# Performance work log

Measured on AMD Instinct MI355X. Metric: run time of the kernel, lower is better.

## Reference

```python
import jax, jax.numpy as jnp
import numpy as np

B, T, C = 4, 2048, 1024
H, D = 16, 64  # n_head, head_dim; H*D == C
EPS = 1e-12


def _l2norm(x):
    # matches torch F.normalize(dim=-1): x / max(||x||_2, eps)
    n = jnp.sqrt(jnp.sum(x * x, axis=-1, keepdims=True))
    return x / jnp.maximum(n, EPS)


def setup_inputs() -> dict:
    key = jax.random.key(0)
    ks = jax.random.split(key, 8)
    s = 0.02
    return {
        "x": jax.random.normal(ks[0], (B, T, C), dtype=jnp.float32),
        "Wq": jax.random.normal(ks[1], (C, C), dtype=jnp.float32) * s,
        "Wk": jax.random.normal(ks[2], (C, C), dtype=jnp.float32) * s,
        "Wv": jax.random.normal(ks[3], (C, C), dtype=jnp.float32) * s,
        "Wbeta": jax.random.normal(ks[4], (H, C), dtype=jnp.float32) * s,
        "bbeta": jnp.zeros((H,), dtype=jnp.float32),
        "Wgate": jax.random.normal(ks[5], (C, C), dtype=jnp.float32) * s,
        "Wo": jax.random.normal(ks[6], (C, C), dtype=jnp.float32) * s,
    }


def _forward(x, Wq, Wk, Wv, Wbeta, bbeta, Wgate, Wo):
    q = (x @ Wq.T).reshape(B, T, H, D)
    k = (x @ Wk.T).reshape(B, T, H, D)
    v = (x @ Wv.T).reshape(B, T, H, D)
    beta = jax.nn.sigmoid(x @ Wbeta.T + bbeta)  # (B,T,H)
    gate = jax.nn.sigmoid(x @ Wgate.T)          # (B,T,C)

    q = _l2norm(q)
    k = _l2norm(k)

    # time-major for scan: (T,B,H,D) / (T,B,H)
    qT = jnp.transpose(q, (1, 0, 2, 3))
    kT = jnp.transpose(k, (1, 0, 2, 3))
    vT = jnp.transpose(v, (1, 0, 2, 3))
    bT = jnp.transpose(beta, (1, 0, 2))

    M0 = jnp.zeros((B, H, D, D), dtype=x.dtype)

    def step(M, inp):
        q_t, k_t, v_t, b_t = inp
        o_t = jnp.einsum('bhdc,bhc->bhd', M, q_t)       # read state with q (pre-update)
        Mk = jnp.einsum('bhdc,bhc->bhd', M, k_t)
        dv = v_t - Mk                                    # delta-rule error
        M = M + b_t[..., None, None] * jnp.einsum('bhd,bhc->bhdc', dv, k_t)
        return M, o_t

    _, oT = jax.lax.scan(step, M0, (qT, kT, vT, bT))     # oT: (T,B,H,D)
    o = jnp.transpose(oT, (1, 0, 2, 3)).reshape(B, T, C)
    return (gate * o) @ Wo.T


def reference(x, Wq, Wk, Wv, Wbeta, bbeta, Wgate, Wo):
    return _forward(x, Wq, Wk, Wv, Wbeta, bbeta, Wgate, Wo)
```

## Files before the change

kernel.cpp:

```cpp
#include <hip/hip_runtime.h>
#include <cstdint>
#include <cstddef>

#define Bz 4
#define Tz 2048
#define Cz 1024
#define Hz 16
#define Dz 64
#define NTOK (Bz*Tz)
#define CHL 32
#define NCH (Tz/CHL)

typedef __attribute__((ext_vector_type(8))) short  short8;
typedef __attribute__((ext_vector_type(4))) float  floatx4;

__device__ __forceinline__ unsigned short f2bf(float x) {
  union { float f; uint32_t u; } a; a.f = x;
  uint32_t r = a.u + 0x7fffu + ((a.u >> 16) & 1u);
  return (unsigned short)(r >> 16);
}
__device__ __forceinline__ float bf2f(unsigned short u) {
  union { uint32_t i; float f; } a; a.i = ((uint32_t)u) << 16; return a.f;
}
__device__ __forceinline__ float sigmoidf_(float z) {
  return 1.0f / (1.0f + __expf(-z));
}

__device__ __forceinline__ void gload_lds16(const void* gptr, void* lptr) {
  __builtin_amdgcn_global_load_lds(
      (const __attribute__((address_space(1))) void*)(uintptr_t)gptr,
      (__attribute__((address_space(3))) void*)(uint32_t)(uintptr_t)lptr,
      16, 0, 0);
}

template<int CTRL>
__device__ __forceinline__ float dpp_addf(float x) {
  int y = __builtin_amdgcn_update_dpp(0, __float_as_int(x), CTRL, 0xF, 0xF, true);
  return x + __int_as_float(y);
}
__device__ __forceinline__ float rowsum16(float x) {
  x = dpp_addf<0xB1>(x);
  x = dpp_addf<0x4E>(x);
  x = dpp_addf<0x124>(x);
  x = dpp_addf<0x128>(x);
  return x;
}

union FragU { uint32_t u[4]; short8 s; };

__global__ __launch_bounds__(256) void cvt_bf16_kernel(const float* __restrict__ in,
                                                       unsigned short* __restrict__ out,
                                                       int n4) {
  int i = blockIdx.x * blockDim.x + threadIdx.x;
  int stride = gridDim.x * blockDim.x;
  const float4* in4 = (const float4*)in;
  ushort4* out4 = (ushort4*)out;
  for (; i < n4; i += stride) {
    float4 f = in4[i];
    ushort4 u;
    u.x = f2bf(f.x); u.y = f2bf(f.y); u.z = f2bf(f.z); u.w = f2bf(f.w);
    out4[i] = u;
  }
}

__global__ __launch_bounds__(256) void cvt_w5_kernel(
    const float* __restrict__ s0, const float* __restrict__ s1,
    const float* __restrict__ s2, const float* __restrict__ s3,
    const float* __restrict__ s4,
    unsigned short* __restrict__ d0, unsigned short* __restrict__ d1,
    unsigned short* __restrict__ d2, unsigned short* __restrict__ d3,
    unsigned short* __restrict__ d4, int n4)
{
  const int w = blockIdx.y;
  const float* s = (w == 0) ? s0 : (w == 1) ? s1 : (w == 2) ? s2 : (w == 3) ? s3 : s4;
  unsigned short* d = (w == 0) ? d0 : (w == 1) ? d1 : (w == 2) ? d2 : (w == 3) ? d3 : d4;
  int i = blockIdx.x * blockDim.x + threadIdx.x;
  if (i < n4) {
    float4 f = ((const float4*)s)[i];
    ushort4 u;
    u.x = f2bf(f.x); u.y = f2bf(f.y); u.z = f2bf(f.z); u.w = f2bf(f.w);
    ((ushort4*)d)[i] = u;
  }
}

__global__ __launch_bounds__(256) void gemm_bt_kernel(
    const unsigned short* __restrict__ A,
    const unsigned short* __restrict__ W0, const unsigned short* __restrict__ W1,
    const unsigned short* __restrict__ W2, const unsigned short* __restrict__ W3,
    void* __restrict__ O0, void* __restrict__ O1,
    void* __restrict__ O2, void* __restrict__ O3,
    int M, int N, int K, int nz_sigmoid, int norm_mask, int out_bf16)
{
  const int z = blockIdx.z;
  const unsigned short* Bw = (z == 0) ? W0 : (z == 1) ? W1 : (z == 2) ? W2 : W3;
  void* Cw = (z == 0) ? O0 : (z == 1) ? O1 : (z == 2) ? O2 : O3;
  const bool act = (z == nz_sigmoid);
  const bool donorm = (norm_mask >> z) & 1;

  __shared__ unsigned short As[128 * 32];
  __shared__ unsigned short Bs[128 * 32];

  const int tid  = threadIdx.x;
  const int wid  = tid >> 6;
  const int lane = tid & 63;
  const int wm = wid & 1, wn = wid >> 1;
  const int m0 = blockIdx.y * 128;
  const int n0 = blockIdx.x * 128;

  const int srow = tid >> 2;
  const int scol = (tid & 3) * 8;

  floatx4 acc[4][4];
#pragma unroll
  for (int i = 0; i < 4; ++i)
#pragma unroll
    for (int j = 0; j < 4; ++j)
      acc[i][j] = floatx4{0.f, 0.f, 0.f, 0.f};

  const int ml = lane & 15;
  const int kq = lane >> 4;

  const unsigned short* Arow0 = A  + (size_t)(m0 + srow) * K + scol;
  const unsigned short* Arow1 = A  + (size_t)(m0 + 64 + srow) * K + scol;
  const unsigned short* Brow0 = Bw + (size_t)(n0 + srow) * K + scol;
  const unsigned short* Brow1 = Bw + (size_t)(n0 + 64 + srow) * K + scol;

  for (int kt = 0; kt < K; kt += 32) {
    gload_lds16(Arow0 + kt, &As[wid * 512]);
    gload_lds16(Arow1 + kt, &As[2048 + wid * 512]);
    gload_lds16(Brow0 + kt, &Bs[wid * 512]);
    gload_lds16(Brow1 + kt, &Bs[2048 + wid * 512]);
    __syncthreads();

    short8 af[4], bfv[4];
#pragma unroll
    for (int i = 0; i < 4; ++i) {
      af[i]  = *(const short8*)&As[(wm * 64 + i * 16 + ml) * 32 + kq * 8];
      bfv[i] = *(const short8*)&Bs[(wn * 64 + i * 16 + ml) * 32 + kq * 8];
    }
#pragma unroll
    for (int i = 0; i < 4; ++i)
#pragma unroll
      for (int j = 0; j < 4; ++j)
        acc[i][j] = __builtin_amdgcn_mfma_f32_16x16x32_bf16(af[i], bfv[j], acc[i][j], 0, 0, 0);
    __syncthreads();
  }

  float scale[4][4];
  if (donorm) {
#pragma unroll
    for (int i = 0; i < 4; ++i) {
#pragma unroll
      for (int r = 0; r < 4; ++r) {
        float ss = 0.f;
#pragma unroll
        for (int j = 0; j < 4; ++j) ss = fmaf(acc[i][j][r], acc[i][j][r], ss);
        ss = rowsum16(ss);
        scale[i][r] = 1.0f / fmaxf(sqrtf(ss), 1e-12f);
      }
    }
  }

  const int row_base = m0 + wm * 64;
  const int col_base = n0 + wn * 64;
#pragma unroll
  for (int i = 0; i < 4; ++i) {
#pragma unroll
    for (int j = 0; j < 4; ++j) {
      int col = col_base + j * 16 + ml;
#pragma unroll
      for (int r = 0; r < 4; ++r) {
        int row = row_base + i * 16 + kq * 4 + r;
        float val = acc[i][j][r];
        if (donorm) val *= scale[i][r];
        if (act) val = sigmoidf_(val);
        if (out_bf16) ((unsigned short*)Cw)[(size_t)row * N + col] = f2bf(val);
        else          ((float*)Cw)[(size_t)row * N + col] = val;
      }
    }
  }
}

__global__ __launch_bounds__(256) void beta_kernel(
    const float* __restrict__ x, const float* __restrict__ Wb,
    const float* __restrict__ bb, float* __restrict__ beta_out)
{
  const int n = blockIdx.x;
  const int wid = threadIdx.x >> 6;
  const int lane = threadIdx.x & 63;
  const float* xr = x + (size_t)n * Cz;
  for (int h = wid; h < Hz; h += 4) {
    const float* wr = Wb + (size_t)h * Cz;
    float s = 0.f;
#pragma unroll 4
    for (int i = lane; i < Cz; i += 64) s = fmaf(xr[i], wr[i], s);
#pragma unroll
    for (int ofs = 32; ofs >= 1; ofs >>= 1) s += __shfl_xor(s, ofs);
    if (lane == 0) beta_out[(size_t)n * Hz + h] = sigmoidf_(s + bb[h]);
  }
}


__global__ __launch_bounds__(256) void deltachunk_phase1(
    const unsigned short* __restrict__ qb, const unsigned short* __restrict__ kb,
    const unsigned short* __restrict__ vb, const float* __restrict__ betaf,
    float* __restrict__ of,
    unsigned short* __restrict__ qtb, unsigned short* __restrict__ wbuf,
    unsigned short* __restrict__ ubuf, unsigned short* __restrict__ ktb)
{
  __shared__ unsigned short Kb[32][72], Qb[32][72], Vb[32][72];
  __shared__ float As[32][33];
  __shared__ unsigned short Sb[32][40];
  __shared__ unsigned short Us[32][72], Ws[32][72], Qts[32][72];
  __shared__ float bsh[32];

  const int bid = blockIdx.x;
  const int chain = bid & 63;
  const int chunk = bid >> 6;
  const int b = chain >> 4, h = chain & 15;
  const int tid = threadIdx.x;
  const int wid = tid >> 6, lane = tid & 63;
  const int ml = lane & 15, kq = lane >> 4;

  const size_t tok0 = (size_t)b * Tz + (size_t)chunk * CHL;
  const size_t cb = ((size_t)chain * NCH + chunk) * 2048;

  {
    const int row = tid >> 3, c8 = (tid & 7) * 8;
    const size_t ga = (tok0 + row) * Cz + h * Dz + c8;
    *(uint4*)&Qb[row][c8] = *(const uint4*)&qb[ga];
    *(uint4*)&Kb[row][c8] = *(const uint4*)&kb[ga];
    *(uint4*)&Vb[row][c8] = *(const uint4*)&vb[ga];
  }
  if (tid < 32) bsh[tid] = betaf[(tok0 + tid) * Hz + h];
  __syncthreads();

  {
    const int tr = wid & 1, tc = wid >> 1;
    floatx4 accA = {0.f,0.f,0.f,0.f}, accS = {0.f,0.f,0.f,0.f};
#pragma unroll
    for (int eh = 0; eh < 2; ++eh) {
      short8 ka = *(const short8*)&Kb[tr * 16 + ml][eh * 32 + kq * 8];
      short8 kbf = *(const short8*)&Kb[tc * 16 + ml][eh * 32 + kq * 8];
      short8 qa = *(const short8*)&Qb[tr * 16 + ml][eh * 32 + kq * 8];
      accA = __builtin_amdgcn_mfma_f32_16x16x32_bf16(ka, kbf, accA, 0, 0, 0);
      accS = __builtin_amdgcn_mfma_f32_16x16x32_bf16(qa, kbf, accS, 0, 0, 0);
    }
#pragma unroll
    for (int r = 0; r < 4; ++r) {
      int t = tr * 16 + kq * 4 + r;
      int s = tc * 16 + ml;
      As[t][s] = bsh[t] * accA[r];
      Sb[t][s] = (t > s) ? f2bf(accS[r]) : (unsigned short)0;
    }
  }
  __syncthreads();

  if (tid < 128) {
    const int j = tid;
    float x[32];
    if (j < 64) {
#pragma unroll
      for (int t = 0; t < 32; ++t) x[t] = bsh[t] * bf2f(Vb[t][j]);
    } else {
#pragma unroll
      for (int t = 0; t < 32; ++t) x[t] = bsh[t] * bf2f(Kb[t][j - 64]);
    }
#pragma unroll
    for (int t = 0; t < 31; ++t) {
      float xt = x[t];
#pragma unroll
      for (int s = t + 1; s < 32; ++s) x[s] = fmaf(-As[s][t], xt, x[s]);
    }
    if (j < 64) {
#pragma unroll
      for (int t = 0; t < 32; ++t) Us[t][j] = f2bf(x[t]);
    } else {
#pragma unroll
      for (int t = 0; t < 32; ++t) Ws[t][j - 64] = f2bf(x[t]);
    }
  }
  __syncthreads();

  {
    const int dw = wid * 16 + ml;
    FragU bu, bw;
#pragma unroll
    for (int r = 0; r < 4; ++r) {
      bu.u[r] = (uint32_t)Us[kq * 8 + 2 * r][dw] | ((uint32_t)Us[kq * 8 + 2 * r + 1][dw] << 16);
      bw.u[r] = (uint32_t)Ws[kq * 8 + 2 * r][dw] | ((uint32_t)Ws[kq * 8 + 2 * r + 1][dw] << 16);
    }
    floatx4 accO[2], accQ[2];
#pragma unroll
    for (int tt = 0; tt < 2; ++tt) { accO[tt] = floatx4{0.f,0.f,0.f,0.f}; accQ[tt] = floatx4{0.f,0.f,0.f,0.f}; }
#pragma unroll
    for (int tt = 0; tt < 2; ++tt) {
      short8 sa = *(const short8*)&Sb[tt * 16 + ml][kq * 8];
      accO[tt] = __builtin_amdgcn_mfma_f32_16x16x32_bf16(sa, bu.s, accO[tt], 0, 0, 0);
      accQ[tt] = __builtin_amdgcn_mfma_f32_16x16x32_bf16(sa, bw.s, accQ[tt], 0, 0, 0);
    }
#pragma unroll
    for (int tt = 0; tt < 2; ++tt) {
#pragma unroll
      for (int r = 0; r < 4; ++r) {
        int t = tt * 16 + kq * 4 + r;
        of[(tok0 + t) * Cz + h * Dz + dw] = accO[tt][r];
        Qts[t][dw] = f2bf(bf2f(Qb[t][dw]) - accQ[tt][r]);
      }
    }
  }

  unsigned short ktmp[8];
  {
    const int e = tid >> 2, tq = (tid & 3) * 8;
#pragma unroll
    for (int i2 = 0; i2 < 8; ++i2) ktmp[i2] = Kb[tq + i2][e];
  }
  __syncthreads();

  {
    const int row = tid >> 3, c8 = (tid & 7) * 8;
    const size_t o16 = cb + (size_t)row * 64 + c8;
    *(uint4*)&qtb[o16]  = *(const uint4*)&Qts[row][c8];
    *(uint4*)&wbuf[o16] = *(const uint4*)&Ws[row][c8];
    *(uint4*)&ubuf[o16] = *(const uint4*)&Us[row][c8];
    const int e = tid >> 2, tq = (tid & 3) * 8;
    *(uint4*)&ktb[cb + (size_t)e * 32 + tq] = *(const uint4*)ktmp;
  }
}

__global__ __launch_bounds__(256) void deltachunk_phase2(
    const unsigned short* __restrict__ qtb, const unsigned short* __restrict__ wbuf,
    const unsigned short* __restrict__ ubuf, const unsigned short* __restrict__ ktb,
    float* __restrict__ of)
{
  __shared__ unsigned short Gb[64][72];
  __shared__ unsigned short Kts[64][40];
  __shared__ unsigned short Ub[32][72];
  __shared__ unsigned short Mh[64][72], Ml[64][72];
  __shared__ unsigned short Zh[64][40], Zl[64][40];

  const int chain = blockIdx.x;
  const int b = chain >> 4, h = chain & 15;
  const int tid = threadIdx.x;
  const int wid = tid >> 6, lane = tid & 63;
  const int ml = lane & 15, kq = lane >> 4;
  const int iq = wid >> 1, jq = wid & 1;
  const int dq = wid >> 1, eq = wid & 1;

  for (int i = tid; i < 64 * 72; i += 256) { (&Mh[0][0])[i] = 0; (&Ml[0][0])[i] = 0; }
  floatx4 mAcc[2][2];
#pragma unroll
  for (int a = 0; a < 2; ++a)
#pragma unroll
    for (int e = 0; e < 2; ++e) mAcc[a][e] = floatx4{0.f,0.f,0.f,0.f};

  const int grow = tid >> 3, gc8 = (tid & 7) * 8;
  const int ke = tid >> 2,  kt8 = (tid & 3) * 8;

  {
    const size_t cb = (size_t)chain * NCH * 2048;
    *(uint4*)&Gb[grow][gc8]      = *(const uint4*)&qtb[cb + (size_t)grow * 64 + gc8];
    *(uint4*)&Gb[32 + grow][gc8] = *(const uint4*)&wbuf[cb + (size_t)grow * 64 + gc8];
    *(uint4*)&Ub[grow][gc8]      = *(const uint4*)&ubuf[cb + (size_t)grow * 64 + gc8];
    *(uint4*)&Kts[ke][kt8]       = *(const uint4*)&ktb[cb + (size_t)ke * 32 + kt8];
  }
  __syncthreads();

  for (int c = 0; c < NCH; ++c) {
    const size_t tok0 = (size_t)b * Tz + (size_t)c * CHL;
    float pre[2][2][4];
    if (iq == 0) {
#pragma unroll
      for (int ti = 0; ti < 2; ++ti)
#pragma unroll
        for (int tj = 0; tj < 2; ++tj)
#pragma unroll
          for (int r = 0; r < 4; ++r)
            pre[ti][tj][r] = of[(tok0 + ti * 16 + kq * 4 + r) * Cz + h * Dz + jq * 32 + tj * 16 + ml];
    }
    const int cn = (c + 1 < NCH) ? c + 1 : c;
    const size_t cbn = ((size_t)chain * NCH + cn) * 2048;
    uint4 sq = *(const uint4*)&qtb[cbn + (size_t)grow * 64 + gc8];
    uint4 sw = *(const uint4*)&wbuf[cbn + (size_t)grow * 64 + gc8];
    uint4 su = *(const uint4*)&ubuf[cbn + (size_t)grow * 64 + gc8];
    uint4 sk = *(const uint4*)&ktb[cbn + (size_t)ke * 32 + kt8];

    __syncthreads();

    floatx4 g1[2][2];
#pragma unroll
    for (int ti = 0; ti < 2; ++ti)
#pragma unroll
      for (int tj = 0; tj < 2; ++tj) g1[ti][tj] = floatx4{0.f,0.f,0.f,0.f};
#pragma unroll
    for (int eh = 0; eh < 2; ++eh) {
      short8 afr[2];
      afr[0] = *(const short8*)&Gb[iq * 32 + 0  + ml][eh * 32 + kq * 8];
      afr[1] = *(const short8*)&Gb[iq * 32 + 16 + ml][eh * 32 + kq * 8];
#pragma unroll
      for (int hl = 0; hl < 2; ++hl) {
#pragma unroll
        for (int tj = 0; tj < 2; ++tj) {
          short8 bfr = hl ? *(const short8*)&Ml[jq * 32 + tj * 16 + ml][eh * 32 + kq * 8]
                          : *(const short8*)&Mh[jq * 32 + tj * 16 + ml][eh * 32 + kq * 8];
          g1[0][tj] = __builtin_amdgcn_mfma_f32_16x16x32_bf16(afr[0], bfr, g1[0][tj], 0, 0, 0);
          g1[1][tj] = __builtin_amdgcn_mfma_f32_16x16x32_bf16(afr[1], bfr, g1[1][tj], 0, 0, 0);
        }
      }
    }
    if (iq == 0) {
#pragma unroll
      for (int ti = 0; ti < 2; ++ti)
#pragma unroll
        for (int tj = 0; tj < 2; ++tj)
#pragma unroll
          for (int r = 0; r < 4; ++r)
            of[(tok0 + ti * 16 + kq * 4 + r) * Cz + h * Dz + jq * 32 + tj * 16 + ml] =
                pre[ti][tj][r] + g1[ti][tj][r];
    } else {
#pragma unroll
      for (int ti = 0; ti < 2; ++ti)
#pragma unroll
        for (int tj = 0; tj < 2; ++tj)
#pragma unroll
          for (int r = 0; r < 4; ++r) {
            int t = ti * 16 + kq * 4 + r, d = jq * 32 + tj * 16 + ml;
            float z = bf2f(Ub[t][d]) - g1[ti][tj][r];
            unsigned short zh = f2bf(z);
            Zh[d][t] = zh;
            Zl[d][t] = f2bf(z - bf2f(zh));
          }
    }
    __syncthreads();

    {
      short8 kfr[2];
      kfr[0] = *(const short8*)&Kts[eq * 32 + 0  + ml][kq * 8];
      kfr[1] = *(const short8*)&Kts[eq * 32 + 16 + ml][kq * 8];
#pragma unroll
      for (int hl = 0; hl < 2; ++hl) {
#pragma unroll
        for (int dt = 0; dt < 2; ++dt) {
          short8 afr = hl ? *(const short8*)&Zl[dq * 32 + dt * 16 + ml][kq * 8]
                          : *(const short8*)&Zh[dq * 32 + dt * 16 + ml][kq * 8];
          mAcc[dt][0] = __builtin_amdgcn_mfma_f32_16x16x32_bf16(afr, kfr[0], mAcc[dt][0], 0, 0, 0);
          mAcc[dt][1] = __builtin_amdgcn_mfma_f32_16x16x32_bf16(afr, kfr[1], mAcc[dt][1], 0, 0, 0);
        }
      }
#pragma unroll
      for (int dt = 0; dt < 2; ++dt)
#pragma unroll
        for (int et = 0; et < 2; ++et)
#pragma unroll
          for (int r = 0; r < 4; ++r) {
            int d = dq * 32 + dt * 16 + kq * 4 + r;
            int ec = eq * 32 + et * 16 + ml;
            float mv = mAcc[dt][et][r];
            unsigned short mh = f2bf(mv);
            Mh[d][ec] = mh;
            Ml[d][ec] = f2bf(mv - bf2f(mh));
          }
    }
    __syncthreads();

    *(uint4*)&Gb[grow][gc8]      = sq;
    *(uint4*)&Gb[32 + grow][gc8] = sw;
    *(uint4*)&Ub[grow][gc8]      = su;
    *(uint4*)&Kts[ke][kt8]       = sk;
  }
}

__global__ __launch_bounds__(256) void gate_mul_kernel(
    const unsigned short* __restrict__ gsig, const float* __restrict__ o,
    unsigned short* __restrict__ out, int n4)
{
  int i = blockIdx.x * blockDim.x + threadIdx.x;
  int stride = gridDim.x * blockDim.x;
  const ushort4* g4 = (const ushort4*)gsig;
  const float4* o4 = (const float4*)o;
  ushort4* out4 = (ushort4*)out;
  for (; i < n4; i += stride) {
    ushort4 gv = g4[i];
    float4 ov = o4[i];
    ushort4 u;
    u.x = f2bf(bf2f(gv.x) * ov.x);
    u.y = f2bf(bf2f(gv.y) * ov.y);
    u.z = f2bf(bf2f(gv.z) * ov.z);
    u.w = f2bf(bf2f(gv.w) * ov.w);
    out4[i] = u;
  }
}

extern "C" void kernel_launch(void* const* d_in, const int* in_sizes, int n_in,
                              void* d_out, int out_size, void* d_ws, size_t ws_size,
                              hipStream_t stream) {
  const float* x     = (const float*)d_in[0];
  const float* Wq    = (const float*)d_in[1];
  const float* Wk    = (const float*)d_in[2];
  const float* Wv    = (const float*)d_in[3];
  const float* Wbeta = (const float*)d_in[4];
  const float* bbeta = (const float*)d_in[5];
  const float* Wgate = (const float*)d_in[6];
  const float* Wo    = (const float*)d_in[7];
  float* out = (float*)d_out;

  char* ws = (char*)d_ws;
  size_t off = 0;
  auto alloc = [&](size_t bytes) -> char* {
    char* p = ws + off;
    off += (bytes + 255) & ~(size_t)255;
    return p;
  };
  unsigned short* xb  = (unsigned short*)alloc((size_t)NTOK * Cz * 2);
  unsigned short* Wqb = (unsigned short*)alloc((size_t)Cz * Cz * 2);
  unsigned short* Wkb = (unsigned short*)alloc((size_t)Cz * Cz * 2);
  unsigned short* Wvb = (unsigned short*)alloc((size_t)Cz * Cz * 2);
  unsigned short* Wgb = (unsigned short*)alloc((size_t)Cz * Cz * 2);
  unsigned short* Wob = (unsigned short*)alloc((size_t)Cz * Cz * 2);
  unsigned short* qb  = (unsigned short*)alloc((size_t)NTOK * Cz * 2);
  unsigned short* kb  = (unsigned short*)alloc((size_t)NTOK * Cz * 2);
  unsigned short* vb  = (unsigned short*)alloc((size_t)NTOK * Cz * 2);
  unsigned short* gb  = (unsigned short*)alloc((size_t)NTOK * Cz * 2);
  float* of    = (float*)alloc((size_t)NTOK * Cz * 4);
  float* betaf = (float*)alloc((size_t)NTOK * Hz * 4);
  unsigned short* qtb  = (unsigned short*)alloc((size_t)64 * NCH * 2048 * 2);
  unsigned short* wbuf = (unsigned short*)alloc((size_t)64 * NCH * 2048 * 2);
  unsigned short* ubuf = (unsigned short*)alloc((size_t)64 * NCH * 2048 * 2);
  unsigned short* ktb  = (unsigned short*)alloc((size_t)64 * NCH * 2048 * 2);
  unsigned short* ab = xb;

  const int n4x = NTOK * Cz / 4;
  const int n4w = Cz * Cz / 4;

  cvt_bf16_kernel<<<dim3(1024), dim3(256), 0, stream>>>(x, xb, n4x);
  cvt_w5_kernel<<<dim3(n4w / 256, 5), dim3(256), 0, stream>>>(
      Wq, Wk, Wv, Wgate, Wo, Wqb, Wkb, Wvb, Wgb, Wob, n4w);

  gemm_bt_kernel<<<dim3(Cz / 128, NTOK / 128, 4), dim3(256), 0, stream>>>(
      xb, Wqb, Wkb, Wvb, Wgb, qb, kb, vb, gb, NTOK, Cz, Cz, 3, 3, 1);

  beta_kernel<<<dim3(NTOK), dim3(256), 0, stream>>>(x, Wbeta, bbeta, betaf);

  deltachunk_phase1<<<dim3(64 * NCH), dim3(256), 0, stream>>>(
      qb, kb, vb, betaf, of, qtb, wbuf, ubuf, ktb);
  deltachunk_phase2<<<dim3(Bz * Hz), dim3(256), 0, stream>>>(qtb, wbuf, ubuf, ktb, of);

  gate_mul_kernel<<<dim3(1024), dim3(256), 0, stream>>>(gb, of, ab, n4x);

  gemm_bt_kernel<<<dim3(Cz / 128, NTOK / 128, 1), dim3(256), 0, stream>>>(
      ab, Wob, Wob, Wob, Wob, out, out, out, out, NTOK, Cz, Cz, -1, 0, 0);
}
```

Baseline: 436.4 us.

## Replace GEMM with 256x256-tile, 8-wave, multi-stage pipelined LDS kernel

Swaps the 128x128 single-buffered bf16 GEMM for a 256x256 tile using 512 threads and a double-buffered LDS ring. Global-to-LDS loads are issued several half-tiles ahead and fenced with explicit vmcnt waits. LDS reads use an XOR swizzle to cut bank conflicts, workgroup IDs are remapped for L2 locality, and MFMA blocks run at raised priority. It targets the load-then-compute stalls of the old kernel and raises data reuse. In exchange it needs many more accumulator registers and much larger LDS per block, and the hand-placed waitcnt/barrier schedule is fragile. The output GEMM now launches only 128 workgroups, which may underfill the GPU.

```diff
diff --git a/kernel.cpp b/kernel.cpp
--- a/kernel.cpp
+++ b/kernel.cpp
@@ -83,7 +83,14 @@
   }
 }
 
-__global__ __launch_bounds__(256) void gemm_bt_kernel(
+
+#define VM8()  asm volatile("s_waitcnt vmcnt(8)" ::: "memory")
+#define VM4()  asm volatile("s_waitcnt vmcnt(4)" ::: "memory")
+#define VM0()  asm volatile("s_waitcnt vmcnt(0)" ::: "memory")
+#define LGKM0() asm volatile("s_waitcnt lgkmcnt(0)" ::: "memory")
+#define BARR() __builtin_amdgcn_s_barrier()
+
+__global__ __launch_bounds__(512, 2) void gemm256_kernel(
     const unsigned short* __restrict__ A,
     const unsigned short* __restrict__ W0, const unsigned short* __restrict__ W1,
     const unsigned short* __restrict__ W2, const unsigned short* __restrict__ W3,
@@ -91,65 +98,115 @@
     void* __restrict__ O2, void* __restrict__ O3,
     int M, int N, int K, int nz_sigmoid, int norm_mask, int out_bf16)
 {
-  const int z = blockIdx.z;
-  const unsigned short* Bw = (z == 0) ? W0 : (z == 1) ? W1 : (z == 2) ? W2 : W3;
-  void* Cw = (z == 0) ? O0 : (z == 1) ? O1 : (z == 2) ? O2 : O3;
-  const bool act = (z == nz_sigmoid);
-  const bool donorm = (norm_mask >> z) & 1;
-
-  __shared__ unsigned short As[128 * 32];
-  __shared__ unsigned short Bs[128 * 32];
-
-  const int tid  = threadIdx.x;
-  const int wid  = tid >> 6;
-  const int lane = tid & 63;
-  const int wm = wid & 1, wn = wid >> 1;
-  const int m0 = blockIdx.y * 128;
-  const int n0 = blockIdx.x * 128;
-
-  const int srow = tid >> 2;
-  const int scol = (tid & 3) * 8;
-
-  floatx4 acc[4][4];
-#pragma unroll
-  for (int i = 0; i < 4; ++i)
-#pragma unroll
-    for (int j = 0; j < 4; ++j)
-      acc[i][j] = floatx4{0.f, 0.f, 0.f, 0.f};
-
-  const int ml = lane & 15;
-  const int kq = lane >> 4;
-
-  const unsigned short* Arow0 = A  + (size_t)(m0 + srow) * K + scol;
-  const unsigned short* Arow1 = A  + (size_t)(m0 + 64 + srow) * K + scol;
-  const unsigned short* Brow0 = Bw + (size_t)(n0 + srow) * K + scol;
-  const unsigned short* Brow1 = Bw + (size_t)(n0 + 64 + srow) * K + scol;
-
-  for (int kt = 0; kt < K; kt += 32) {
-    gload_lds16(Arow0 + kt, &As[wid * 512]);
-    gload_lds16(Arow1 + kt, &As[2048 + wid * 512]);
-    gload_lds16(Brow0 + kt, &Bs[wid * 512]);
-    gload_lds16(Brow1 + kt, &Bs[2048 + wid * 512]);
-    __syncthreads();
-
-    short8 af[4], bfv[4];
-#pragma unroll
-    for (int i = 0; i < 4; ++i) {
-      af[i]  = *(const short8*)&As[(wm * 64 + i * 16 + ml) * 32 + kq * 8];
-      bfv[i] = *(const short8*)&Bs[(wn * 64 + i * 16 + ml) * 32 + kq * 8];
-    }
-#pragma unroll
-    for (int i = 0; i < 4; ++i)
-#pragma unroll
-      for (int j = 0; j < 4; ++j)
-        acc[i][j] = __builtin_amdgcn_mfma_f32_16x16x32_bf16(af[i], bfv[j], acc[i][j], 0, 0, 0);
-    __syncthreads();
-  }
-
-  float scale[4][4];
+  __shared__ unsigned short smem[8 * 8192];
+
+  const int gx = gridDim.x, gz = gridDim.z;
+  const int nwg = gx * gridDim.y * gz;
+  int flat = (blockIdx.z * gridDim.y + blockIdx.y) * gx + blockIdx.x;
+  if ((nwg & 7) == 0) flat = (flat & 7) * (nwg >> 3) + (flat >> 3);
+  const int xz = gx * gz;
+  const int by = flat / xz;
+  const int rem = flat - by * xz;
+  const int bz = rem / gx;
+  const int bx = rem - bz * gx;
+
+  const unsigned short* Bw = (bz == 0) ? W0 : (bz == 1) ? W1 : (bz == 2) ? W2 : W3;
+  void* Cw = (bz == 0) ? O0 : (bz == 1) ? O1 : (bz == 2) ? O2 : O3;
+  const bool act = (bz == nz_sigmoid);
+  const bool donorm = (norm_mask >> bz) & 1;
+
+  const int m0 = by * 256, n0 = bx * 256;
+  const int tid = threadIdx.x;
+  const int wid = tid >> 6, lane = tid & 63;
+  const int wm = wid >> 2, wn = wid & 3;
+  const int ml = lane & 15, kq = lane >> 4;
+
+  const unsigned short* Ap = A  + (size_t)m0 * K;
+  const unsigned short* Bp = Bw + (size_t)n0 * K;
+
+  const int srow = wid * 16 + (lane >> 2);
+  const int ss8  = ((lane & 3) ^ ((lane >> 3) & 3)) * 8;
+
+  const int rs8  = (kq ^ ((ml >> 1) & 3)) * 8;
+  const int arow = wm * 128 + ml;
+  const int brow = wn * 64 + ml;
+
+  const int NT = K >> 6;
+  const int hmax = NT << 2;
+
+  floatx4 acc[8][4];
+#pragma unroll
+  for (int i = 0; i < 8; ++i)
+#pragma unroll
+    for (int j = 0; j < 4; ++j) acc[i][j] = floatx4{0.f, 0.f, 0.f, 0.f};
+
+#define STAGE1(hsi) do {                                                      \
+    const int ht_ = (hsi) >> 2, hh_ = (hsi) & 3;                              \
+    const unsigned short* p_ = (hh_ & 1) ? Bp : Ap;                           \
+    const int kb_ = ht_ * 64 + (hh_ >> 1) * 32;                               \
+    unsigned short* lb_ = &smem[(((ht_ & 1) << 2) + hh_) * 8192 + wid * 512]; \
+    gload_lds16(p_ + (size_t)srow * K + kb_ + ss8, lb_);                      \
+    gload_lds16(p_ + (size_t)(128 + srow) * K + kb_ + ss8, lb_ + 4096);       \
+  } while (0)
+
+  int hs = 0;
+  for (; hs < 6 && hs < hmax; ++hs) STAGE1(hs);
+  VM8();
+  BARR();
+
+#define LOAD_A(Hb, mh)                                                        \
+  _Pragma("unroll") for (int i = 0; i < 4; ++i)                               \
+    af[i] = *(const short8*)&Hb[(arow + (mh) * 64 + i * 16) * 32 + rs8];
+#define LOAD_B(Hb)                                                            \
+  _Pragma("unroll") for (int j = 0; j < 4; ++j)                               \
+    bf[j] = *(const short8*)&Hb[(brow + j * 16) * 32 + rs8];
+#define MFMA_Q(mh)                                                            \
+  __builtin_amdgcn_s_setprio(1);                                              \
+  _Pragma("unroll") for (int i = 0; i < 4; ++i)                               \
+    _Pragma("unroll") for (int j = 0; j < 4; ++j)                             \
+      acc[(mh) * 4 + i][j] = __builtin_amdgcn_mfma_f32_16x16x32_bf16(         \
+          af[i], bf[j], acc[(mh) * 4 + i][j], 0, 0, 0);                       \
+  __builtin_amdgcn_s_setprio(0);
+#define STAGE_NEXT() do { if (hs < hmax) { STAGE1(hs); ++hs; } } while (0)
+
+  short8 af[4], bf[4];
+  for (int t = 0; t < NT; ++t) {
+    const unsigned short* Ah0 = &smem[(((t & 1) << 2) + 0) * 8192];
+    const unsigned short* Bh0 = &smem[(((t & 1) << 2) + 1) * 8192];
+    const unsigned short* Ah1 = &smem[(((t & 1) << 2) + 2) * 8192];
+    const unsigned short* Bh1 = &smem[(((t & 1) << 2) + 3) * 8192];
+
+    LOAD_A(Ah0, 0); LOAD_B(Bh0);
+    STAGE_NEXT();
+    BARR(); LGKM0();
+    MFMA_Q(0);
+    BARR();
+
+    LOAD_A(Ah0, 1);
+    STAGE_NEXT();
+    BARR(); LGKM0();
+    MFMA_Q(1);
+    if (t == NT - 1) { VM0(); } else { VM8(); }
+    BARR();
+
+    LOAD_A(Ah1, 0); LOAD_B(Bh1);
+    STAGE_NEXT();
+    BARR(); LGKM0();
+    MFMA_Q(0);
+    BARR();
+
+    LOAD_A(Ah1, 1);
+    STAGE_NEXT();
+    BARR(); LGKM0();
+    MFMA_Q(1);
+    if (t < NT - 2) { VM8(); } else if (t == NT - 2) { VM4(); }
+    BARR();
+  }
+
+  float scale[8][4];
   if (donorm) {
 #pragma unroll
-    for (int i = 0; i < 4; ++i) {
+    for (int i = 0; i < 8; ++i) {
 #pragma unroll
       for (int r = 0; r < 4; ++r) {
         float ss = 0.f;
@@ -161,16 +218,16 @@
     }
   }
 
-  const int row_base = m0 + wm * 64;
+  const int row_base = m0 + wm * 128;
   const int col_base = n0 + wn * 64;
 #pragma unroll
-  for (int i = 0; i < 4; ++i) {
+  for (int i = 0; i < 8; ++i) {
 #pragma unroll
     for (int j = 0; j < 4; ++j) {
-      int col = col_base + j * 16 + ml;
+      const int col = col_base + j * 16 + ml;
 #pragma unroll
       for (int r = 0; r < 4; ++r) {
-        int row = row_base + i * 16 + kq * 4 + r;
+        const int row = row_base + i * 16 + kq * 4 + r;
         float val = acc[i][j][r];
         if (donorm) val *= scale[i][r];
         if (act) val = sigmoidf_(val);
@@ -199,7 +256,6 @@
     if (lane == 0) beta_out[(size_t)n * Hz + h] = sigmoidf_(s + bb[h]);
   }
 }
-
 
 __global__ __launch_bounds__(256) void deltachunk_phase1(
     const unsigned short* __restrict__ qb, const unsigned short* __restrict__ kb,
@@ -537,7 +593,7 @@
   cvt_w5_kernel<<<dim3(n4w / 256, 5), dim3(256), 0, stream>>>(
       Wq, Wk, Wv, Wgate, Wo, Wqb, Wkb, Wvb, Wgb, Wob, n4w);
 
-  gemm_bt_kernel<<<dim3(Cz / 128, NTOK / 128, 4), dim3(256), 0, stream>>>(
+  gemm256_kernel<<<dim3(Cz / 256, NTOK / 256, 4), dim3(512), 0, stream>>>(
       xb, Wqb, Wkb, Wvb, Wgb, qb, kb, vb, gb, NTOK, Cz, Cz, 3, 3, 1);
 
   beta_kernel<<<dim3(NTOK), dim3(256), 0, stream>>>(x, Wbeta, bbeta, betaf);
@@ -548,6 +604,6 @@
 
   gate_mul_kernel<<<dim3(1024), dim3(256), 0, stream>>>(gb, of, ab, n4x);
 
-  gemm_bt_kernel<<<dim3(Cz / 128, NTOK / 128, 1), dim3(256), 0, stream>>>(
+  gemm256_kernel<<<dim3(Cz / 256, NTOK / 256, 1), dim3(512), 0, stream>>>(
       ab, Wob, Wob, Wob, Wob, out, out, out, out, NTOK, Cz, Cz, -1, 0, 0);
 }
```

Measured after the change: 417.5 us. 4.3% less time.
